# Performance work log

Hardware: AMD Instinct MI355X
Metric: run time of the kernel (lower is better)

Reference implementation:

```python
import jax, jax.numpy as jnp
import numpy as np

N_OPT, OUT_F, IN_F = 16, 1024, 1024
B, A = 8, 512


def setup_inputs() -> dict:
    key = jax.random.key(0)
    k1, k2, k3, k4 = jax.random.split(key, 4)
    x = jax.random.normal(k1, (B, A, IN_F), dtype=jnp.float32)
    sp = jax.random.uniform(k2, (B, N_OPT), dtype=jnp.float32)
    selection_probs = sp / jnp.sum(sp, axis=-1, keepdims=True)
    # kaiming-uniform-ish init scale
    bound_w = 1.0 / np.sqrt(IN_F)
    weight = jax.random.uniform(k3, (N_OPT, OUT_F, IN_F), dtype=jnp.float32,
                                minval=-bound_w, maxval=bound_w)
    bias = jax.random.uniform(k4, (N_OPT, OUT_F), dtype=jnp.float32,
                              minval=-bound_w, maxval=bound_w)
    return {"x": x, "selection_probs": selection_probs, "weight": weight, "bias": bias}


def reference(x, selection_probs, weight, bias):
    # Math identical to torch forward:
    #   transformed = einsum('nij,baj->bani', weight, x)
    #   out = einsum('bani,bn->bai', transformed, selection_probs)
    # reassociated efficiently: mix weights per-example first, then one batched matmul.
    w_mixed = jnp.einsum('nij,bn->bij', weight, selection_probs)   # [B, out, in]
    out = jnp.einsum('bij,baj->bai', w_mixed, x)                   # [B, A, out]
    b_mixed = jnp.einsum('ni,bn->bi', bias, selection_probs)       # [B, out]
    return out + b_mixed[:, None, :]
```

## Files before the change

### kernel.cpp

```cpp
#include <hip/hip_runtime.h>
#include <hip/hip_bf16.h>


#define B_SZ 8
#define A_SZ 512
#define IN_F 1024
#define OUT_F 1024
#define N_OPT 16

typedef short short8 __attribute__((ext_vector_type(8)));
typedef float floatx4 __attribute__((ext_vector_type(4)));

__device__ __forceinline__ unsigned short f2bf(float f) {
    unsigned int u = __builtin_bit_cast(unsigned int, f);
    u += 0x7fffu + ((u >> 16) & 1u);
    return (unsigned short)(u >> 16);
}

#define GLOBAL_LOAD_LDS16(g, l)                                                    \
    __builtin_amdgcn_global_load_lds(                                              \
        (const __attribute__((address_space(1))) void*)(g),                        \
        (__attribute__((address_space(3))) void*)(l), 16, 0, 0)

__global__ __launch_bounds__(256) void selin_prep(
    const float* __restrict__ x, const float* __restrict__ sp,
    const float* __restrict__ weight, const float* __restrict__ bias,
    unsigned short* __restrict__ wm, unsigned short* __restrict__ xbf,
    float* __restrict__ bmixed)
{
    const int bid = blockIdx.x;
    const int tid = threadIdx.x;

    if (bid < 1024) {
        __shared__ float sps[B_SZ * N_OPT];
        if (tid < B_SZ * N_OPT) sps[tid] = sp[tid];
        __syncthreads();
        const int e4 = bid * 256 + tid;
        const float4* w4 = (const float4*)weight;
        float4 w[N_OPT];
#pragma unroll
        for (int n = 0; n < N_OPT; n++)
            w[n] = w4[(size_t)n * (IN_F * OUT_F / 4) + e4];
#pragma unroll
        for (int b = 0; b < B_SZ; b++) {
            float ax = 0.f, ay = 0.f, az = 0.f, aw = 0.f;
#pragma unroll
            for (int n = 0; n < N_OPT; n++) {
                float s = sps[b * N_OPT + n];
                ax += s * w[n].x; ay += s * w[n].y;
                az += s * w[n].z; aw += s * w[n].w;
            }
            ushort4 o = make_ushort4(f2bf(ax), f2bf(ay), f2bf(az), f2bf(aw));
            ((ushort4*)wm)[(size_t)b * (IN_F * OUT_F / 4) + e4] = o;
        }
#pragma unroll
        for (int j = 0; j < 4; j++) {
            const int idx = bid * 1024 + j * 256 + tid;
            float4 v = ((const float4*)x)[idx];
            ((ushort4*)xbf)[idx] =
                make_ushort4(f2bf(v.x), f2bf(v.y), f2bf(v.z), f2bf(v.w));
        }
    } else {
        __shared__ float sps[B_SZ * N_OPT];
        if (tid < B_SZ * N_OPT) sps[tid] = sp[tid];
        __syncthreads();
        const int idx = (bid - 1024) * 256 + tid;
        const int b = idx >> 8, i4 = idx & 255;
        const float4* bias4 = (const float4*)bias;
        float ax = 0.f, ay = 0.f, az = 0.f, aw = 0.f;
#pragma unroll
        for (int n = 0; n < N_OPT; n++) {
            float s = sps[b * N_OPT + n];
            float4 v = bias4[n * 256 + i4];
            ax += s * v.x; ay += s * v.y; az += s * v.z; aw += s * v.w;
        }
        ((float4*)bmixed)[idx] = make_float4(ax, ay, az, aw);
    }
}

__global__ __launch_bounds__(256) void selin_gemm(
    const unsigned short* __restrict__ xbf, const unsigned short* __restrict__ wm,
    const float* __restrict__ bmixed, float* __restrict__ out)
{
    __shared__ __align__(16) unsigned short As[2][64 * 32];
    __shared__ __align__(16) unsigned short Bs[2][64 * 32];

    const int tid = threadIdx.x;
    const int bid = blockIdx.x;
    const int b   = bid & 7;
    const int t   = bid >> 3;
    const int mb  = t & 7;
    const int nb  = t >> 3;
    const int m0  = mb * 64, n0 = nb * 64;

    const unsigned short* Ag = xbf + ((size_t)b * A_SZ  + m0) * IN_F;
    const unsigned short* Bg = wm  + ((size_t)b * OUT_F + n0) * IN_F;

    const int ga = (tid >> 2) * IN_F + (tid & 3) * 8;

    const int lane = tid & 63;
    const int wv   = tid >> 6;
    const int wmi  = wv >> 1, wni = wv & 1;
    const int lm   = lane & 15, kq = lane >> 4;

    floatx4 acc[2][2];
#pragma unroll
    for (int i = 0; i < 2; i++)
#pragma unroll
        for (int j = 0; j < 2; j++)
            acc[i][j] = (floatx4){0.f, 0.f, 0.f, 0.f};

    for (int k0 = 0; k0 < IN_F; k0 += 64) {
        GLOBAL_LOAD_LDS16(Ag + ga + k0,      &As[0][tid * 8]);
        GLOBAL_LOAD_LDS16(Ag + ga + k0 + 32, &As[1][tid * 8]);
        GLOBAL_LOAD_LDS16(Bg + ga + k0,      &Bs[0][tid * 8]);
        GLOBAL_LOAD_LDS16(Bg + ga + k0 + 32, &Bs[1][tid * 8]);
        __syncthreads();

#pragma unroll
        for (int kh = 0; kh < 2; kh++) {
            short8 a[2], bb[2];
#pragma unroll
            for (int mi = 0; mi < 2; mi++)
                a[mi] = *(const short8*)&As[kh][(wmi * 32 + mi * 16 + lm) * 32 + kq * 8];
#pragma unroll
            for (int ni = 0; ni < 2; ni++)
                bb[ni] = *(const short8*)&Bs[kh][(wni * 32 + ni * 16 + lm) * 32 + kq * 8];

#pragma unroll
            for (int mi = 0; mi < 2; mi++)
#pragma unroll
                for (int ni = 0; ni < 2; ni++)
                    acc[mi][ni] = __builtin_amdgcn_mfma_f32_16x16x32_bf16(
                        a[mi], bb[ni], acc[mi][ni], 0, 0, 0);
        }
        __syncthreads();
    }

#pragma unroll
    for (int ni = 0; ni < 2; ni++) {
        const int gcol = n0 + wni * 32 + ni * 16 + lm;
        const float bv = bmixed[b * OUT_F + gcol];
#pragma unroll
        for (int mi = 0; mi < 2; mi++) {
            const int grow = m0 + wmi * 32 + mi * 16 + kq * 4;
            float* op = out + ((size_t)b * A_SZ + grow) * OUT_F + gcol;
#pragma unroll
            for (int r = 0; r < 4; r++)
                op[(size_t)r * OUT_F] = acc[mi][ni][r] + bv;
        }
    }
}

extern "C" void kernel_launch(void* const* d_in, const int* in_sizes, int n_in,
                              void* d_out, int out_size, void* d_ws, size_t ws_size,
                              hipStream_t stream) {
    const float* x      = (const float*)d_in[0];
    const float* sp     = (const float*)d_in[1];
    const float* weight = (const float*)d_in[2];
    const float* bias   = (const float*)d_in[3];
    float* out = (float*)d_out;

    unsigned short* wm  = (unsigned short*)d_ws;
    unsigned short* xbf = wm + (size_t)B_SZ * OUT_F * IN_F;
    float* bmixed       = (float*)(xbf + (size_t)B_SZ * A_SZ * IN_F);

    selin_prep<<<1032, 256, 0, stream>>>(x, sp, weight, bias, wm, xbf, bmixed);
    selin_gemm<<<1024, 256, 0, stream>>>(xbf, wm, bmixed, out);
}
```

Baseline: 130.2 us.

## Pre-swizzle bf16 activations into MFMA fragment layout and load A directly to registers

The prep kernel now writes x as bf16 in a k-chunk-major layout where each 8-element k slice for a row is contiguous, so each lane's MFMA A fragment is one 16-byte global load. The GEMM drops the A tile from LDS and reads A fragments straight from global/L2 into registers before the barrier, cutting LDS traffic and shared memory use. In exchange, A data is no longer shared across waves through LDS: the two waves with the same wmi each load the same fragments, and the transposed writes in prep are scattered.

```diff
diff --git a/kernel.cpp b/kernel.cpp
--- a/kernel.cpp
+++ b/kernel.cpp
@@ -25,7 +25,7 @@
 __global__ __launch_bounds__(256) void selin_prep(
     const float* __restrict__ x, const float* __restrict__ sp,
     const float* __restrict__ weight, const float* __restrict__ bias,
-    unsigned short* __restrict__ wm, unsigned short* __restrict__ xbf,
+    unsigned short* __restrict__ wm, unsigned short* __restrict__ xt,
     float* __restrict__ bmixed)
 {
     const int bid = blockIdx.x;
@@ -53,12 +53,22 @@
             ushort4 o = make_ushort4(f2bf(ax), f2bf(ay), f2bf(az), f2bf(aw));
             ((ushort4*)wm)[(size_t)b * (IN_F * OUT_F / 4) + e4] = o;
         }
+        const float4* x4 = (const float4*)x;
 #pragma unroll
-        for (int j = 0; j < 4; j++) {
-            const int idx = bid * 1024 + j * 256 + tid;
-            float4 v = ((const float4*)x)[idx];
-            ((ushort4*)xbf)[idx] =
-                make_ushort4(f2bf(v.x), f2bf(v.y), f2bf(v.z), f2bf(v.w));
+        for (int j = 0; j < 2; j++) {
+            const int g  = bid * 256 + tid + j * 262144;
+            const int wg = g >> 6, l = g & 63;
+            const int b  = wg >> 10, rem = wg & 1023;
+            const int r  = ((rem & 31) << 4) + (l & 15);
+            const int c  = ((rem >> 5) << 2) + (l >> 4);
+            const size_t ridx = ((size_t)(b * 512 + r)) * 256 + c * 2;
+            float4 v0 = x4[ridx], v1 = x4[ridx + 1];
+            short8 o;
+            o[0] = (short)f2bf(v0.x); o[1] = (short)f2bf(v0.y);
+            o[2] = (short)f2bf(v0.z); o[3] = (short)f2bf(v0.w);
+            o[4] = (short)f2bf(v1.x); o[5] = (short)f2bf(v1.y);
+            o[6] = (short)f2bf(v1.z); o[7] = (short)f2bf(v1.w);
+            *(short8*)(xt + ((size_t)b * 65536 + (size_t)c * 512 + r) * 8) = o;
         }
     } else {
         __shared__ float sps[B_SZ * N_OPT];
@@ -79,10 +89,9 @@
 }
 
 __global__ __launch_bounds__(256) void selin_gemm(
-    const unsigned short* __restrict__ xbf, const unsigned short* __restrict__ wm,
+    const unsigned short* __restrict__ xt, const unsigned short* __restrict__ wm,
     const float* __restrict__ bmixed, float* __restrict__ out)
 {
-    __shared__ __align__(16) unsigned short As[2][64 * 32];
     __shared__ __align__(16) unsigned short Bs[2][64 * 32];
 
     const int tid = threadIdx.x;
@@ -93,15 +102,19 @@
     const int nb  = t >> 3;
     const int m0  = mb * 64, n0 = nb * 64;
 
-    const unsigned short* Ag = xbf + ((size_t)b * A_SZ  + m0) * IN_F;
-    const unsigned short* Bg = wm  + ((size_t)b * OUT_F + n0) * IN_F;
-
+    const unsigned short* Bg = wm + ((size_t)b * OUT_F + n0) * IN_F;
     const int ga = (tid >> 2) * IN_F + (tid & 3) * 8;
 
     const int lane = tid & 63;
     const int wv   = tid >> 6;
     const int wmi  = wv >> 1, wni = wv & 1;
     const int lm   = lane & 15, kq = lane >> 4;
+
+    const unsigned short* xtb = xt + (size_t)b * 524288;
+    const unsigned short* ap[2];
+#pragma unroll
+    for (int mi = 0; mi < 2; mi++)
+        ap[mi] = xtb + (size_t)kq * 4096 + (size_t)(m0 + wmi * 32 + mi * 16 + lm) * 8;
 
     floatx4 acc[2][2];
 #pragma unroll
@@ -110,29 +123,32 @@
         for (int j = 0; j < 2; j++)
             acc[i][j] = (floatx4){0.f, 0.f, 0.f, 0.f};
 
-    for (int k0 = 0; k0 < IN_F; k0 += 64) {
-        GLOBAL_LOAD_LDS16(Ag + ga + k0,      &As[0][tid * 8]);
-        GLOBAL_LOAD_LDS16(Ag + ga + k0 + 32, &As[1][tid * 8]);
+    for (int it = 0; it < 16; it++) {
+        const int k0 = it * 64;
         GLOBAL_LOAD_LDS16(Bg + ga + k0,      &Bs[0][tid * 8]);
         GLOBAL_LOAD_LDS16(Bg + ga + k0 + 32, &Bs[1][tid * 8]);
+
+        short8 a[2][2];
+        const size_t coff = (size_t)it * 32768;
+#pragma unroll
+        for (int mi = 0; mi < 2; mi++) {
+            a[mi][0] = *(const short8*)(ap[mi] + coff);
+            a[mi][1] = *(const short8*)(ap[mi] + coff + 16384);
+        }
         __syncthreads();
 
 #pragma unroll
         for (int kh = 0; kh < 2; kh++) {
-            short8 a[2], bb[2];
-#pragma unroll
-            for (int mi = 0; mi < 2; mi++)
-                a[mi] = *(const short8*)&As[kh][(wmi * 32 + mi * 16 + lm) * 32 + kq * 8];
+            short8 bb[2];
 #pragma unroll
             for (int ni = 0; ni < 2; ni++)
                 bb[ni] = *(const short8*)&Bs[kh][(wni * 32 + ni * 16 + lm) * 32 + kq * 8];
-
 #pragma unroll
             for (int mi = 0; mi < 2; mi++)
 #pragma unroll
                 for (int ni = 0; ni < 2; ni++)
                     acc[mi][ni] = __builtin_amdgcn_mfma_f32_16x16x32_bf16(
-                        a[mi], bb[ni], acc[mi][ni], 0, 0, 0);
+                        a[mi][kh], bb[ni], acc[mi][ni], 0, 0, 0);
         }
         __syncthreads();
     }
@@ -162,9 +178,9 @@
     float* out = (float*)d_out;
 
     unsigned short* wm  = (unsigned short*)d_ws;
-    unsigned short* xbf = wm + (size_t)B_SZ * OUT_F * IN_F;
-    float* bmixed       = (float*)(xbf + (size_t)B_SZ * A_SZ * IN_F);
+    unsigned short* xt  = wm + (size_t)B_SZ * OUT_F * IN_F;
+    float* bmixed       = (float*)(xt + (size_t)B_SZ * A_SZ * IN_F);
 
-    selin_prep<<<1032, 256, 0, stream>>>(x, sp, weight, bias, wm, xbf, bmixed);
-    selin_gemm<<<1024, 256, 0, stream>>>(xbf, wm, bmixed, out);
+    selin_prep<<<1032, 256, 0, stream>>>(x, sp, weight, bias, wm, xt, bmixed);
+    selin_gemm<<<1024, 256, 0, stream>>>(xt, wm, bmixed, out);
 }
```

Result: slower. 133.6 us (+2.6%).
